# Performance work log

Hardware: AMD Instinct MI355X
Metric: run time of the kernel (lower is better)

The kernel has to match this reference:

```python
import jax, jax.numpy as jnp
import numpy as np

N = 40000   # num_words
H = 384     # hidden_dim
D = 20000   # num_docs
E = 800000  # word-word edges
NNZ = 800000  # doc-word tfidf entries
ALPHA = 0.65
EPS = 1e-5


def layernorm(x, g, b):
    m = jnp.mean(x, axis=-1, keepdims=True)
    v = jnp.mean((x - m) ** 2, axis=-1, keepdims=True)
    return (x - m) * jax.lax.rsqrt(v + EPS) * g + b


def gelu(x):
    return jax.nn.gelu(x, approximate=False)  # torch F.gelu default (erf)


def spmm(rows, cols, vals, M, n_out):
    # COO sparse [n_out, n_in] @ dense [n_in, H]
    return jax.ops.segment_sum(vals[:, None] * M[cols], rows, num_segments=n_out)


def setup_inputs() -> dict:
    key = jax.random.key(0)
    ks = jax.random.split(key, 24)
    s = 1.0 / np.sqrt(H)
    inp = {
        "A_rows": jax.random.randint(ks[0], (E,), 0, N, dtype=jnp.int32),
        "A_cols": jax.random.randint(ks[1], (E,), 0, N, dtype=jnp.int32),
        "A_vals": jax.random.uniform(ks[2], (E,), jnp.float32),
        "X_rows": jax.random.randint(ks[3], (NNZ,), 0, D, dtype=jnp.int32),
        "X_cols": jax.random.randint(ks[4], (NNZ,), 0, N, dtype=jnp.int32),
        "X_vals": jax.random.uniform(ks[5], (NNZ,), jnp.float32),
        "num_docs": D,
        "emb": jax.random.normal(ks[6], (N, H), jnp.float32) * s,
        "W1": jax.random.normal(ks[7], (H, H), jnp.float32) * s,
        "W2": jax.random.normal(ks[8], (H, H), jnp.float32) * s,
        "W3": jax.random.normal(ks[9], (H, H), jnp.float32) * s,
        "g1": jnp.ones((H,), jnp.float32), "b1": jnp.zeros((H,), jnp.float32),
        "g2": jnp.ones((H,), jnp.float32), "b2": jnp.zeros((H,), jnp.float32),
        "g3": jnp.ones((H,), jnp.float32), "b3": jnp.zeros((H,), jnp.float32),
        "mlp_W1": jax.random.normal(ks[10], (H, H), jnp.float32) * s,
        "mlp_b1": jnp.zeros((H,), jnp.float32),
        "mlp_g": jnp.ones((H,), jnp.float32), "mlp_bn": jnp.zeros((H,), jnp.float32),
        "mlp_W2": jax.random.normal(ks[11], (H, H // 2), jnp.float32) * s,
        "mlp_b2": jnp.zeros((H // 2,), jnp.float32),
        "cls_W": jax.random.normal(ks[12], (H // 2, 2), jnp.float32) * s,
        "cls_b": jnp.zeros((2,), jnp.float32),
        "gate_W1": jax.random.normal(ks[13], (2 * H, H), jnp.float32) * s,
        "gate_b1": jnp.zeros((H,), jnp.float32),
        "gate_W2": jax.random.normal(ks[14], (H, H), jnp.float32) * s,
        "gate_b2": jnp.zeros((H,), jnp.float32),
    }
    return inp


def reference(A_rows, A_cols, A_vals, X_rows, X_cols, X_vals, num_docs, emb,
              W1, W2, W3, g1, b1, g2, b2, g3, b3,
              mlp_W1, mlp_b1, mlp_g, mlp_bn, mlp_W2, mlp_b2,
              cls_W, cls_b, gate_W1, gate_b1, gate_W2, gate_b2):
    n = emb.shape[0]
    # --- 3 residual GCN blocks over word graph (eval mode: dropout off) ---
    h = spmm(A_rows, A_cols, A_vals, emb, n)
    h = gelu(layernorm(h @ W1, g1, b1))
    h = spmm(A_rows, A_cols, A_vals, h, n)
    h = gelu(layernorm(h @ W2, g2, b2))
    h = spmm(A_rows, A_cols, A_vals, h, n)
    h = gelu(layernorm(h @ W3, g3, b3))
    word_H = (1.0 - ALPHA) * emb + ALPHA * h
    # --- doc aggregation via TF-IDF SpMM ---
    doc_H = spmm(X_rows, X_cols, X_vals, word_H, num_docs)
    doc_H0 = spmm(X_rows, X_cols, X_vals, emb, num_docs)
    gate_in = jnp.concatenate([doc_H, doc_H0], axis=1)
    gate = jax.nn.sigmoid(gelu(gate_in @ gate_W1 + gate_b1) @ gate_W2 + gate_b2)
    doc = gate * doc_H + (1.0 - gate) * doc_H0
    # --- MLP head ---
    doc = layernorm(gelu(doc @ mlp_W1 + mlp_b1), mlp_g, mlp_bn)
    doc = gelu(doc @ mlp_W2 + mlp_b2)
    logits = doc @ cls_W + cls_b
    return logits
```

## Files before the change

### kernel.cpp

```cpp
#include <hip/hip_runtime.h>
#include <hip/hip_fp16.h>

#define HD 384
#define HHD 192
#define TPR 96
#define RPB 4
#define ECHUNK 128

using bf16x8 = __attribute__((ext_vector_type(8))) short;
using f32x4  = __attribute__((ext_vector_type(4))) float;

__device__ __forceinline__ float gelu_f(float x) {
    return 0.5f * x * (1.0f + erff(x * 0.70710678118654752f));
}

__device__ __forceinline__ float sigmoid_f(float x) {
    return 1.0f / (1.0f + expf(-x));
}

__device__ __forceinline__ void ld_h4(const __half2* p, float2& lo, float2& hi) {
    uint2 raw = *reinterpret_cast<const uint2*>(p);
    lo = __half22float2(*reinterpret_cast<const __half2*>(&raw.x));
    hi = __half22float2(*reinterpret_cast<const __half2*>(&raw.y));
}

__global__ __launch_bounds__(256) void hist_rows(
        const int* __restrict__ rows, int* __restrict__ cnt, int nnz) {
    int e = blockIdx.x * blockDim.x + threadIdx.x;
    if (e < nnz) atomicAdd(&cnt[rows[e]], 1);
}

__global__ __launch_bounds__(256) void scan_local(
        const int* __restrict__ cnt, int* __restrict__ rp,
        int* __restrict__ bsum, int n) {
    __shared__ int wsum[4];
    int i = blockIdx.x * 256 + threadIdx.x;
    int lane = threadIdx.x & 63, wv = threadIdx.x >> 6;
    int v = (i < n) ? cnt[i] : 0;
    int s = v;
    #pragma unroll
    for (int o = 1; o < 64; o <<= 1) {
        int t = __shfl_up(s, o);
        if (lane >= o) s += t;
    }
    if (lane == 63) wsum[wv] = s;
    __syncthreads();
    int woff = 0;
    for (int w = 0; w < wv; ++w) woff += wsum[w];
    if (i < n) rp[i] = woff + s - v;
    if (threadIdx.x == 255) bsum[blockIdx.x] = woff + s;
}

__global__ __launch_bounds__(256) void scan_bsums(
        const int* __restrict__ bsum, int* __restrict__ boff,
        int nb, int* __restrict__ total_out) {
    __shared__ int tmp[256];
    int tid = threadIdx.x;
    int v = (tid < nb) ? bsum[tid] : 0;
    tmp[tid] = v;
    __syncthreads();
    for (int o = 1; o < 256; o <<= 1) {
        int t = (tid >= o) ? tmp[tid - o] : 0;
        __syncthreads();
        tmp[tid] += t;
        __syncthreads();
    }
    if (tid < nb) boff[tid] = tmp[tid] - v;
    if (tid == nb - 1) *total_out = tmp[tid];
}

__global__ __launch_bounds__(256) void scan_add(
        int* __restrict__ rp, const int* __restrict__ boff, int n) {
    int i = blockIdx.x * 256 + threadIdx.x;
    if (i < n) rp[i] += boff[i >> 8];
}

__global__ __launch_bounds__(256) void csr_scatter(
        const int* __restrict__ rows, const int* __restrict__ cols,
        const float* __restrict__ vals, const int* __restrict__ rp,
        int* __restrict__ fill, int* __restrict__ cp,
        float* __restrict__ vp, int nnz) {
    int e = blockIdx.x * blockDim.x + threadIdx.x;
    if (e >= nnz) return;
    int r = rows[e];
    int pos = rp[r] + atomicAdd(&fill[r], 1);
    cp[pos] = cols[e];
    vp[pos] = vals[e];
}

__global__ __launch_bounds__(256) void cvt_fp16(
        const float* __restrict__ in, __half2* __restrict__ out, int n2) {
    int i = blockIdx.x * blockDim.x + threadIdx.x;
    if (i >= n2) return;
    float2 v = reinterpret_cast<const float2*>(in)[i];
    out[i] = __floats2half2_rn(v.x, v.y);
}

__global__ __launch_bounds__(384) void spmm_h2(
        const int* __restrict__ rp, const int* __restrict__ cp,
        const float* __restrict__ vp, const __half2* __restrict__ in,
        __half2* __restrict__ out, int nrows) {
    __shared__ int   lc[RPB][ECHUNK];
    __shared__ float lv[RPB][ECHUNK];
    __shared__ int maxlen_s;
    const int rr = threadIdx.x / TPR;
    const int t  = threadIdx.x % TPR;
    const int r  = blockIdx.x * RPB + rr;
    int s = 0, len = 0;
    if (r < nrows) { s = rp[r]; len = rp[r + 1] - s; }
    if (threadIdx.x == 0) maxlen_s = 0;
    __syncthreads();
    if (t == 0) atomicMax(&maxlen_s, len);
    __syncthreads();
    const int nch = (maxlen_s + ECHUNK - 1) / ECHUNK;
    float a0 = 0.f, a1 = 0.f, a2 = 0.f, a3 = 0.f;
    for (int ch = 0; ch < nch; ++ch) {
        const int base = ch * ECHUNK;
        const int tile = min(ECHUNK, len - base);
        for (int i = t; i < tile; i += TPR) {
            lc[rr][i] = cp[s + base + i];
            lv[rr][i] = vp[s + base + i];
        }
        __syncthreads();
        int p = 0;
        for (; p + 4 <= tile; p += 4) {
            int   c0 = lc[rr][p],     c1 = lc[rr][p + 1];
            int   c2 = lc[rr][p + 2], c3 = lc[rr][p + 3];
            float v0 = lv[rr][p],     v1 = lv[rr][p + 1];
            float v2 = lv[rr][p + 2], v3 = lv[rr][p + 3];
            float2 x0l, x0h, x1l, x1h, x2l, x2h, x3l, x3h;
            ld_h4(in + (size_t)c0 * HHD + 2 * t, x0l, x0h);
            ld_h4(in + (size_t)c1 * HHD + 2 * t, x1l, x1h);
            ld_h4(in + (size_t)c2 * HHD + 2 * t, x2l, x2h);
            ld_h4(in + (size_t)c3 * HHD + 2 * t, x3l, x3h);
            a0 = fmaf(v0, x0l.x, a0); a1 = fmaf(v0, x0l.y, a1);
            a2 = fmaf(v0, x0h.x, a2); a3 = fmaf(v0, x0h.y, a3);
            a0 = fmaf(v1, x1l.x, a0); a1 = fmaf(v1, x1l.y, a1);
            a2 = fmaf(v1, x1h.x, a2); a3 = fmaf(v1, x1h.y, a3);
            a0 = fmaf(v2, x2l.x, a0); a1 = fmaf(v2, x2l.y, a1);
            a2 = fmaf(v2, x2h.x, a2); a3 = fmaf(v2, x2h.y, a3);
            a0 = fmaf(v3, x3l.x, a0); a1 = fmaf(v3, x3l.y, a1);
            a2 = fmaf(v3, x3h.x, a2); a3 = fmaf(v3, x3h.y, a3);
        }
        for (; p < tile; ++p) {
            int c = lc[rr][p];
            float v = lv[rr][p];
            float2 xl, xh;
            ld_h4(in + (size_t)c * HHD + 2 * t, xl, xh);
            a0 = fmaf(v, xl.x, a0); a1 = fmaf(v, xl.y, a1);
            a2 = fmaf(v, xh.x, a2); a3 = fmaf(v, xh.y, a3);
        }
        __syncthreads();
    }
    if (r < nrows) {
        __half2 o0 = __floats2half2_rn(a0, a1);
        __half2 o1 = __floats2half2_rn(a2, a3);
        uint2 packed;
        packed.x = *reinterpret_cast<unsigned*>(&o0);
        packed.y = *reinterpret_cast<unsigned*>(&o1);
        *reinterpret_cast<uint2*>(out + (size_t)r * HHD + 2 * t) = packed;
    }
}

__global__ __launch_bounds__(384) void spmm_doc2(
        const int* __restrict__ rp, const int* __restrict__ cp,
        const float* __restrict__ vp,
        const __half2* __restrict__ inH, const __half2* __restrict__ inE,
        float* __restrict__ docH, float* __restrict__ docH0, int nrows) {
    __shared__ int   lc[RPB][ECHUNK];
    __shared__ float lv[RPB][ECHUNK];
    __shared__ int maxlen_s;
    const int rr = threadIdx.x / TPR;
    const int t  = threadIdx.x % TPR;
    const int r  = blockIdx.x * RPB + rr;
    int s = 0, len = 0;
    if (r < nrows) { s = rp[r]; len = rp[r + 1] - s; }
    if (threadIdx.x == 0) maxlen_s = 0;
    __syncthreads();
    if (t == 0) atomicMax(&maxlen_s, len);
    __syncthreads();
    const int nch = (maxlen_s + ECHUNK - 1) / ECHUNK;
    float h0 = 0.f, h1 = 0.f, h2 = 0.f, h3 = 0.f;
    float e0 = 0.f, e1 = 0.f, e2 = 0.f, e3 = 0.f;
    for (int ch = 0; ch < nch; ++ch) {
        const int base = ch * ECHUNK;
        const int tile = min(ECHUNK, len - base);
        for (int i = t; i < tile; i += TPR) {
            lc[rr][i] = cp[s + base + i];
            lv[rr][i] = vp[s + base + i];
        }
        __syncthreads();
        int p = 0;
        for (; p + 2 <= tile; p += 2) {
            int   c0 = lc[rr][p], c1 = lc[rr][p + 1];
            float v0 = lv[rr][p], v1 = lv[rr][p + 1];
            float2 ha0, hb0, ea0, eb0, ha1, hb1, ea1, eb1;
            ld_h4(inH + (size_t)c0 * HHD + 2 * t, ha0, hb0);
            ld_h4(inE + (size_t)c0 * HHD + 2 * t, ea0, eb0);
            ld_h4(inH + (size_t)c1 * HHD + 2 * t, ha1, hb1);
            ld_h4(inE + (size_t)c1 * HHD + 2 * t, ea1, eb1);
            h0 = fmaf(v0, ha0.x, h0); h1 = fmaf(v0, ha0.y, h1);
            h2 = fmaf(v0, hb0.x, h2); h3 = fmaf(v0, hb0.y, h3);
            e0 = fmaf(v0, ea0.x, e0); e1 = fmaf(v0, ea0.y, e1);
            e2 = fmaf(v0, eb0.x, e2); e3 = fmaf(v0, eb0.y, e3);
            h0 = fmaf(v1, ha1.x, h0); h1 = fmaf(v1, ha1.y, h1);
            h2 = fmaf(v1, hb1.x, h2); h3 = fmaf(v1, hb1.y, h3);
            e0 = fmaf(v1, ea1.x, e0); e1 = fmaf(v1, ea1.y, e1);
            e2 = fmaf(v1, eb1.x, e2); e3 = fmaf(v1, eb1.y, e3);
        }
        for (; p < tile; ++p) {
            int c = lc[rr][p];
            float v = lv[rr][p];
            float2 ha, hb, ea, eb;
            ld_h4(inH + (size_t)c * HHD + 2 * t, ha, hb);
            ld_h4(inE + (size_t)c * HHD + 2 * t, ea, eb);
            h0 = fmaf(v, ha.x, h0); h1 = fmaf(v, ha.y, h1);
            h2 = fmaf(v, hb.x, h2); h3 = fmaf(v, hb.y, h3);
            e0 = fmaf(v, ea.x, e0); e1 = fmaf(v, ea.y, e1);
            e2 = fmaf(v, eb.x, e2); e3 = fmaf(v, eb.y, e3);
        }
        __syncthreads();
    }
    if (r < nrows) {
        float4 ev = make_float4(e0, e1, e2, e3);
        float4 hv = make_float4(0.35f * e0 + 0.65f * h0, 0.35f * e1 + 0.65f * h1,
                                0.35f * e2 + 0.65f * h2, 0.35f * e3 + 0.65f * h3);
        *reinterpret_cast<float4*>(docH0 + (size_t)r * HD + 4 * t) = ev;
        *reinterpret_cast<float4*>(docH  + (size_t)r * HD + 4 * t) = hv;
    }
}

__global__ __launch_bounds__(256) void pack_w(
        const float* __restrict__ W, unsigned short* __restrict__ out,
        int KS, int NS, int N) {
    int t = blockIdx.x * 256 + threadIdx.x;
    int total = KS * NS * 64;
    if (t >= total) return;
    int l = t & 63;
    int ns = (t >> 6) % NS;
    int ks = t / (64 * NS);
    int col = ns * 16 + (l & 15);
    int k0 = ks * 32 + 8 * (l >> 4);
    size_t obase = (size_t)t * 8;
    size_t pstride = (size_t)KS * NS * 512;
    #pragma unroll
    for (int e = 0; e < 8; ++e) {
        float f = W[(size_t)(k0 + e) * N + col];
        unsigned u = __float_as_uint(f);
        unsigned short h = (unsigned short)(u >> 16);
        float r = f - __uint_as_float(u & 0xFFFF0000u);
        unsigned short lo = (unsigned short)(__float_as_uint(r) >> 16);
        out[obase + e] = (unsigned short)h;
        out[pstride + obase + e] = lo;
    }
}

__device__ __forceinline__ void splitf(const float* f, bf16x8& h, bf16x8& l) {
    #pragma unroll
    for (int e = 0; e < 8; ++e) {
        unsigned u = __float_as_uint(f[e]);
        h[e] = (short)(unsigned short)(u >> 16);
        float r = f[e] - __uint_as_float(u & 0xFFFF0000u);
        l[e] = (short)(unsigned short)(__float_as_uint(r) >> 16);
    }
}

template<int MODE, int NS, int KS, int KSPLIT, bool A16, bool OUT16>
__global__ __launch_bounds__(256) void gemm_mfma(
        const float* __restrict__ A1, const float* __restrict__ A2,
        const unsigned short* __restrict__ Wp,
        const float* __restrict__ bias, const float* __restrict__ gamma,
        const float* __restrict__ beta,
        const float* __restrict__ aux1, const float* __restrict__ aux2,
        float* __restrict__ out, int M) {
    constexpr int N = NS * 16;
    constexpr int NSW = NS / 4;
    const int tid = threadIdx.x;
    const int wave = tid >> 6, l = tid & 63;
    const int row_base = blockIdx.x * 16;
    const int arow = row_base + (l & 15);
    const bool arow_ok = arow < M;
    const int koff = 8 * (l >> 4);
    const size_t pstride = (size_t)KS * NS * 512;

    __shared__ float ps[4][16], pq[4][16];
    __shared__ float mean_s[16], rstd_s[16];
    __shared__ float plg[4][16][2];

    f32x4 acc[NSW];
    #pragma unroll
    for (int ns = 0; ns < NSW; ++ns)
        acc[ns] = f32x4{0.f, 0.f, 0.f, 0.f};

    for (int ks = 0; ks < KS; ++ks) {
        const float* Ap;
        int ksl;
        if (ks < KSPLIT) { Ap = A1; ksl = ks; }
        else             { Ap = A2; ksl = ks - KSPLIT; }
        bf16x8 ah, al;
        if (arow_ok) {
            float f[8];
            if constexpr (A16) {
                const __half2* src = reinterpret_cast<const __half2*>(Ap)
                                     + ((size_t)arow * HD + ksl * 32 + koff) / 2;
                #pragma unroll
                for (int e = 0; e < 4; ++e) {
                    float2 v = __half22float2(src[e]);
                    f[2 * e]     = v.x;
                    f[2 * e + 1] = v.y;
                }
            } else {
                const float* src = Ap + (size_t)arow * HD + ksl * 32 + koff;
                float4 a0 = *reinterpret_cast<const float4*>(src);
                float4 a1 = *reinterpret_cast<const float4*>(src + 4);
                f[0] = a0.x; f[1] = a0.y; f[2] = a0.z; f[3] = a0.w;
                f[4] = a1.x; f[5] = a1.y; f[6] = a1.z; f[7] = a1.w;
            }
            splitf(f, ah, al);
        } else {
            #pragma unroll
            for (int e = 0; e < 8; ++e) { ah[e] = 0; al[e] = 0; }
        }
        const unsigned short* Bp = Wp + (size_t)ks * NS * 512
                                   + (size_t)wave * NSW * 512 + (size_t)l * 8;
        #pragma unroll
        for (int ns = 0; ns < NSW; ++ns) {
            bf16x8 bh = *reinterpret_cast<const bf16x8*>(Bp + ns * 512);
            bf16x8 bl = *reinterpret_cast<const bf16x8*>(Bp + pstride + ns * 512);
            acc[ns] = __builtin_amdgcn_mfma_f32_16x16x32_bf16(ah, bh, acc[ns], 0, 0, 0);
            acc[ns] = __builtin_amdgcn_mfma_f32_16x16x32_bf16(al, bh, acc[ns], 0, 0, 0);
            acc[ns] = __builtin_amdgcn_mfma_f32_16x16x32_bf16(ah, bl, acc[ns], 0, 0, 0);
        }
    }

    const int col_lane = l & 15;
    const int g4 = (l >> 4) * 4;
    constexpr float invN = 1.0f / (float)N;

    if constexpr (MODE == 0 || MODE == 3) {
        if constexpr (MODE == 3) {
            #pragma unroll
            for (int ns = 0; ns < NSW; ++ns) {
                float bb = bias[(wave * NSW + ns) * 16 + col_lane];
                #pragma unroll
                for (int r = 0; r < 4; ++r)
                    acc[ns][r] = gelu_f(acc[ns][r] + bb);
            }
        }
        float s[4] = {0.f, 0.f, 0.f, 0.f}, q[4] = {0.f, 0.f, 0.f, 0.f};
        #pragma unroll
        for (int ns = 0; ns < NSW; ++ns)
            #pragma unroll
            for (int r = 0; r < 4; ++r) {
                float v = acc[ns][r];
                s[r] += v;
                q[r] += v * v;
            }
        #pragma unroll
        for (int r = 0; r < 4; ++r) {
            #pragma unroll
            for (int m = 1; m < 16; m <<= 1) {
                s[r] += __shfl_xor(s[r], m);
                q[r] += __shfl_xor(q[r], m);
            }
        }
        if (col_lane == 0) {
            #pragma unroll
            for (int r = 0; r < 4; ++r) {
                ps[wave][g4 + r] = s[r];
                pq[wave][g4 + r] = q[r];
            }
        }
        __syncthreads();
        if (tid < 16) {
            float ss = ps[0][tid] + ps[1][tid] + ps[2][tid] + ps[3][tid];
            float qq = pq[0][tid] + pq[1][tid] + pq[2][tid] + pq[3][tid];
            float m = ss * invN;
            mean_s[tid] = m;
            rstd_s[tid] = rsqrtf(qq * invN - m * m + 1e-5f);
        }
        __syncthreads();
        #pragma unroll
        for (int ns = 0; ns < NSW; ++ns) {
            int col = (wave * NSW + ns) * 16 + col_lane;
            float gg = gamma[col], bb = beta[col];
            #pragma unroll
            for (int r = 0; r < 4; ++r) {
                int row = row_base + g4 + r;
                if (row < M) {
                    float y = (acc[ns][r] - mean_s[g4 + r]) * rstd_s[g4 + r] * gg + bb;
                    if constexpr (MODE == 0) {
                        y = gelu_f(y);
                        if constexpr (OUT16)
                            reinterpret_cast<__half*>(out)[(size_t)row * N + col] =
                                __float2half(y);
                        else
                            out[(size_t)row * N + col] = y;
                    } else {
                        out[(size_t)row * N + col] = y;
                    }
                }
            }
        }
    } else if constexpr (MODE == 1) {
        #pragma unroll
        for (int ns = 0; ns < NSW; ++ns) {
            int col = (wave * NSW + ns) * 16 + col_lane;
            float bb = bias[col];
            #pragma unroll
            for (int r = 0; r < 4; ++r) {
                int row = row_base + g4 + r;
                if (row < M)
                    out[(size_t)row * N + col] = gelu_f(acc[ns][r] + bb);
            }
        }
    } else if constexpr (MODE == 2) {
        #pragma unroll
        for (int ns = 0; ns < NSW; ++ns) {
            int col = (wave * NSW + ns) * 16 + col_lane;
            float bb = bias[col];
            #pragma unroll
            for (int r = 0; r < 4; ++r) {
                int row = row_base + g4 + r;
                if (row < M) {
                    float g = sigmoid_f(acc[ns][r] + bb);
                    float h1 = aux1[(size_t)row * N + col];
                    float h0 = aux2[(size_t)row * N + col];
                    out[(size_t)row * N + col] = g * h1 + (1.0f - g) * h0;
                }
            }
        }
    } else if constexpr (MODE == 4) {
        float lg0[4] = {0.f, 0.f, 0.f, 0.f}, lg1[4] = {0.f, 0.f, 0.f, 0.f};
        #pragma unroll
        for (int ns = 0; ns < NSW; ++ns) {
            int col = (wave * NSW + ns) * 16 + col_lane;
            float bb = bias[col];
            float c0 = aux1[col * 2 + 0];
            float c1 = aux1[col * 2 + 1];
            #pragma unroll
            for (int r = 0; r < 4; ++r) {
                float v = gelu_f(acc[ns][r] + bb);
                lg0[r] = fmaf(v, c0, lg0[r]);
                lg1[r] = fmaf(v, c1, lg1[r]);
            }
        }
        #pragma unroll
        for (int r = 0; r < 4; ++r) {
            #pragma unroll
            for (int m = 1; m < 16; m <<= 1) {
                lg0[r] += __shfl_xor(lg0[r], m);
                lg1[r] += __shfl_xor(lg1[r], m);
            }
        }
        if (col_lane == 0) {
            #pragma unroll
            for (int r = 0; r < 4; ++r) {
                plg[wave][g4 + r][0] = lg0[r];
                plg[wave][g4 + r][1] = lg1[r];
            }
        }
        __syncthreads();
        if (tid < 32) {
            int rloc = tid >> 1, c = tid & 1;
            int row = row_base + rloc;
            if (row < M) {
                float t = plg[0][rloc][c] + plg[1][rloc][c]
                        + plg[2][rloc][c] + plg[3][rloc][c];
                out[(size_t)row * 2 + c] = t + gamma[c];
            }
        }
    }
}

static void build_csr(const int* rows, const int* cols, const float* vals,
                      int nnz, int n, int* rp, int* cp, float* vp,
                      int* cnt, int* bsum, int* boff, hipStream_t stream) {
    hipMemsetAsync(cnt, 0, (size_t)n * sizeof(int), stream);
    hist_rows<<<(nnz + 255) / 256, 256, 0, stream>>>(rows, cnt, nnz);
    int nb = (n + 255) / 256;
    scan_local<<<nb, 256, 0, stream>>>(cnt, rp, bsum, n);
    scan_bsums<<<1, 256, 0, stream>>>(bsum, boff, nb, rp + n);
    scan_add<<<nb, 256, 0, stream>>>(rp, boff, n);
    hipMemsetAsync(cnt, 0, (size_t)n * sizeof(int), stream);
    csr_scatter<<<(nnz + 255) / 256, 256, 0, stream>>>(rows, cols, vals, rp, cnt, cp, vp, nnz);
}

extern "C" void kernel_launch(void* const* d_in, const int* in_sizes, int n_in,
                              void* d_out, int out_size, void* d_ws, size_t ws_size,
                              hipStream_t stream) {
    const int*   A_rows = (const int*)  d_in[0];
    const int*   A_cols = (const int*)  d_in[1];
    const float* A_vals = (const float*)d_in[2];
    const int*   X_rows = (const int*)  d_in[3];
    const int*   X_cols = (const int*)  d_in[4];
    const float* X_vals = (const float*)d_in[5];
    const float* emb    = (const float*)d_in[7];
    const float* W1     = (const float*)d_in[8];
    const float* W2     = (const float*)d_in[9];
    const float* W3     = (const float*)d_in[10];
    const float* g1     = (const float*)d_in[11];
    const float* b1     = (const float*)d_in[12];
    const float* g2     = (const float*)d_in[13];
    const float* b2     = (const float*)d_in[14];
    const float* g3     = (const float*)d_in[15];
    const float* b3     = (const float*)d_in[16];
    const float* mW1    = (const float*)d_in[17];
    const float* mb1    = (const float*)d_in[18];
    const float* mg     = (const float*)d_in[19];
    const float* mbn    = (const float*)d_in[20];
    const float* mW2    = (const float*)d_in[21];
    const float* mb2    = (const float*)d_in[22];
    const float* cW     = (const float*)d_in[23];
    const float* cb     = (const float*)d_in[24];
    const float* gW1    = (const float*)d_in[25];
    const float* gb1    = (const float*)d_in[26];
    const float* gW2    = (const float*)d_in[27];
    const float* gb2    = (const float*)d_in[28];

    const int E_   = in_sizes[0];
    const int NNZ_ = in_sizes[3];
    const int N_   = in_sizes[7] / HD;
    const int D_   = out_size / 2;

    __half2* emb16 = (__half2*)d_ws;
    __half2* Ba    = emb16 + (size_t)N_ * HHD;
    __half2* Bb    = Ba    + (size_t)N_ * HHD;
    float* docH0 = (float*)(Bb + (size_t)N_ * HHD);
    int*   A_rp = (int*)(docH0 + (size_t)D_ * HD);
    int*   A_cp = A_rp + (N_ + 1);
    float* A_vp = (float*)(A_cp + E_);
    int*   X_rp = (int*)(A_vp + E_);
    int*   X_cp = X_rp + (D_ + 1);
    float* X_vp = (float*)(X_cp + NNZ_);
    int*   cnt  = (int*)(X_vp + NNZ_);
    int*   bsum = cnt + N_;
    int*   boff = bsum + 256;
    size_t pk_off = ((size_t)(boff + 256 - (int*)d_ws) + 7) & ~(size_t)7;
    unsigned short* packs = (unsigned short*)((float*)d_ws + pk_off);
    const size_t SZ_SQ = (size_t)2 * HD * HD;
    unsigned short* p_W1  = packs;
    unsigned short* p_W2  = p_W1  + SZ_SQ;
    unsigned short* p_W3  = p_W2  + SZ_SQ;
    unsigned short* p_gW2 = p_W3  + SZ_SQ;
    unsigned short* p_mW1 = p_gW2 + SZ_SQ;
    unsigned short* p_gW1 = p_mW1 + SZ_SQ;
    unsigned short* p_mW2 = p_gW1 + (size_t)2 * 2 * HD * HD;

    float* docH  = (float*)Ba;
    float* t1    = (float*)emb16;
    float* dmix  = (float*)Bb;
    float* un    = (float*)Ba;
    float* logits = (float*)d_out;

    const int word_grid = (N_ + 15) / 16;
    const int doc_grid  = (D_ + 15) / 16;
    const int spmm_word_grid = (N_ + RPB - 1) / RPB;
    const int spmm_doc_grid  = (D_ + RPB - 1) / RPB;

    pack_w<<<(12 * 24 * 64 + 255) / 256, 256, 0, stream>>>(W1,  p_W1,  12, 24, HD);
    pack_w<<<(12 * 24 * 64 + 255) / 256, 256, 0, stream>>>(W2,  p_W2,  12, 24, HD);
    pack_w<<<(12 * 24 * 64 + 255) / 256, 256, 0, stream>>>(W3,  p_W3,  12, 24, HD);
    pack_w<<<(12 * 24 * 64 + 255) / 256, 256, 0, stream>>>(gW2, p_gW2, 12, 24, HD);
    pack_w<<<(12 * 24 * 64 + 255) / 256, 256, 0, stream>>>(mW1, p_mW1, 12, 24, HD);
    pack_w<<<(24 * 24 * 64 + 255) / 256, 256, 0, stream>>>(gW1, p_gW1, 24, 24, HD);
    pack_w<<<(12 * 12 * 64 + 255) / 256, 256, 0, stream>>>(mW2, p_mW2, 12, 12, HHD);

    cvt_fp16<<<((N_ * HHD) + 255) / 256, 256, 0, stream>>>(emb, emb16, N_ * HHD);

    build_csr(A_rows, A_cols, A_vals, E_, N_, A_rp, A_cp, A_vp, cnt, bsum, boff, stream);
    build_csr(X_rows, X_cols, X_vals, NNZ_, D_, X_rp, X_cp, X_vp, cnt, bsum, boff, stream);

    spmm_h2<<<spmm_word_grid, 384, 0, stream>>>(A_rp, A_cp, A_vp, emb16, Ba, N_);
    gemm_mfma<0, 24, 12, 12, true, true><<<word_grid, 256, 0, stream>>>(
        (const float*)Ba, nullptr, p_W1, nullptr, g1, b1, nullptr, nullptr, (float*)Bb, N_);
    spmm_h2<<<spmm_word_grid, 384, 0, stream>>>(A_rp, A_cp, A_vp, Bb, Ba, N_);
    gemm_mfma<0, 24, 12, 12, true, true><<<word_grid, 256, 0, stream>>>(
        (const float*)Ba, nullptr, p_W2, nullptr, g2, b2, nullptr, nullptr, (float*)Bb, N_);
    spmm_h2<<<spmm_word_grid, 384, 0, stream>>>(A_rp, A_cp, A_vp, Bb, Ba, N_);
    gemm_mfma<0, 24, 12, 12, true, true><<<word_grid, 256, 0, stream>>>(
        (const float*)Ba, nullptr, p_W3, nullptr, g3, b3, nullptr, nullptr, (float*)Bb, N_);

    spmm_doc2<<<spmm_doc_grid, 384, 0, stream>>>(X_rp, X_cp, X_vp, Bb, emb16,
                                                 docH, docH0, D_);

    gemm_mfma<1, 24, 24, 12, false, false><<<doc_grid, 256, 0, stream>>>(
        docH, docH0, p_gW1, gb1, nullptr, nullptr, nullptr, nullptr, t1, D_);
    gemm_mfma<2, 24, 12, 12, false, false><<<doc_grid, 256, 0, stream>>>(
        t1, nullptr, p_gW2, gb2, nullptr, nullptr, docH, docH0, dmix, D_);
    gemm_mfma<3, 24, 12, 12, false, false><<<doc_grid, 256, 0, stream>>>(
        dmix, nullptr, p_mW1, mb1, mg, mbn, nullptr, nullptr, un, D_);
    gemm_mfma<4, 12, 12, 12, false, false><<<doc_grid, 256, 0, stream>>>(
        un, nullptr, p_mW2, mb2, cb, nullptr, cW, nullptr, logits, D_);
}
```

Measured before the change: 1.129 ms.

## Process two 16-row M tiles per block in word-graph GEMMs to reuse B fragments

Adds an MT template parameter so each GEMM block computes MT 16-row tiles, sharing each loaded packed-weight fragment across several A tiles. The three word-graph GEMMs use MT=2 with half the grid, while the doc-side GEMMs stay at MT=1. This aims to halve weight-fragment global/L2 traffic per output row, at the cost of more accumulator registers (possible occupancy loss) and fewer blocks.

```diff
diff --git a/kernel.cpp b/kernel.cpp
--- a/kernel.cpp
+++ b/kernel.cpp
@@ -265,7 +265,30 @@
     }
 }
 
-template<int MODE, int NS, int KS, int KSPLIT, bool A16, bool OUT16>
+template<bool A16>
+__device__ __forceinline__ void load_afrag(
+        const float* Ap, int arow, int ksl, int koff, bf16x8& ah, bf16x8& al) {
+    float f[8];
+    if constexpr (A16) {
+        const __half2* src = reinterpret_cast<const __half2*>(Ap)
+                             + ((size_t)arow * HD + ksl * 32 + koff) / 2;
+        #pragma unroll
+        for (int e = 0; e < 4; ++e) {
+            float2 v = __half22float2(src[e]);
+            f[2 * e]     = v.x;
+            f[2 * e + 1] = v.y;
+        }
+    } else {
+        const float* src = Ap + (size_t)arow * HD + ksl * 32 + koff;
+        float4 a0 = *reinterpret_cast<const float4*>(src);
+        float4 a1 = *reinterpret_cast<const float4*>(src + 4);
+        f[0] = a0.x; f[1] = a0.y; f[2] = a0.z; f[3] = a0.w;
+        f[4] = a1.x; f[5] = a1.y; f[6] = a1.z; f[7] = a1.w;
+    }
+    splitf(f, ah, al);
+}
+
+template<int MODE, int NS, int KS, int KSPLIT, bool A16, bool OUT16, int MT>
 __global__ __launch_bounds__(256) void gemm_mfma(
         const float* __restrict__ A1, const float* __restrict__ A2,
         const unsigned short* __restrict__ Wp,
@@ -277,49 +300,43 @@
     constexpr int NSW = NS / 4;
     const int tid = threadIdx.x;
     const int wave = tid >> 6, l = tid & 63;
-    const int row_base = blockIdx.x * 16;
-    const int arow = row_base + (l & 15);
-    const bool arow_ok = arow < M;
+    const int row_base = blockIdx.x * (16 * MT);
     const int koff = 8 * (l >> 4);
     const size_t pstride = (size_t)KS * NS * 512;
 
-    __shared__ float ps[4][16], pq[4][16];
-    __shared__ float mean_s[16], rstd_s[16];
-    __shared__ float plg[4][16][2];
-
-    f32x4 acc[NSW];
+    __shared__ float ps[4][16 * MT], pq[4][16 * MT];
+    __shared__ float mean_s[16 * MT], rstd_s[16 * MT];
+    __shared__ float plg[4][16 * MT][2];
+
+    int arow[MT];
+    bool aok[MT];
     #pragma unroll
-    for (int ns = 0; ns < NSW; ++ns)
-        acc[ns] = f32x4{0.f, 0.f, 0.f, 0.f};
+    for (int mt = 0; mt < MT; ++mt) {
+        arow[mt] = row_base + mt * 16 + (l & 15);
+        aok[mt] = arow[mt] < M;
+    }
+
+    f32x4 acc[MT][NSW];
+    #pragma unroll
+    for (int mt = 0; mt < MT; ++mt)
+        #pragma unroll
+        for (int ns = 0; ns < NSW; ++ns)
+            acc[mt][ns] = f32x4{0.f, 0.f, 0.f, 0.f};
 
     for (int ks = 0; ks < KS; ++ks) {
         const float* Ap;
         int ksl;
         if (ks < KSPLIT) { Ap = A1; ksl = ks; }
         else             { Ap = A2; ksl = ks - KSPLIT; }
-        bf16x8 ah, al;
-        if (arow_ok) {
-            float f[8];
-            if constexpr (A16) {
-                const __half2* src = reinterpret_cast<const __half2*>(Ap)
-                                     + ((size_t)arow * HD + ksl * 32 + koff) / 2;
-                #pragma unroll
-                for (int e = 0; e < 4; ++e) {
-                    float2 v = __half22float2(src[e]);
-                    f[2 * e]     = v.x;
-                    f[2 * e + 1] = v.y;
-                }
+        bf16x8 ah[MT], al[MT];
+        #pragma unroll
+        for (int mt = 0; mt < MT; ++mt) {
+            if (aok[mt]) {
+                load_afrag<A16>(Ap, arow[mt], ksl, koff, ah[mt], al[mt]);
             } else {
-                const float* src = Ap + (size_t)arow * HD + ksl * 32 + koff;
-                float4 a0 = *reinterpret_cast<const float4*>(src);
-                float4 a1 = *reinterpret_cast<const float4*>(src + 4);
-                f[0] = a0.x; f[1] = a0.y; f[2] = a0.z; f[3] = a0.w;
-                f[4] = a1.x; f[5] = a1.y; f[6] = a1.z; f[7] = a1.w;
-            }
-            splitf(f, ah, al);
-        } else {
-            #pragma unroll
-            for (int e = 0; e < 8; ++e) { ah[e] = 0; al[e] = 0; }
+                #pragma unroll
+                for (int e = 0; e < 8; ++e) { ah[mt][e] = 0; al[mt][e] = 0; }
+            }
         }
         const unsigned short* Bp = Wp + (size_t)ks * NS * 512
                                    + (size_t)wave * NSW * 512 + (size_t)l * 8;
@@ -327,9 +344,12 @@
         for (int ns = 0; ns < NSW; ++ns) {
             bf16x8 bh = *reinterpret_cast<const bf16x8*>(Bp + ns * 512);
             bf16x8 bl = *reinterpret_cast<const bf16x8*>(Bp + pstride + ns * 512);
-            acc[ns] = __builtin_amdgcn_mfma_f32_16x16x32_bf16(ah, bh, acc[ns], 0, 0, 0);
-            acc[ns] = __builtin_amdgcn_mfma_f32_16x16x32_bf16(al, bh, acc[ns], 0, 0, 0);
-            acc[ns] = __builtin_amdgcn_mfma_f32_16x16x32_bf16(ah, bl, acc[ns], 0, 0, 0);
+            #pragma unroll
+            for (int mt = 0; mt < MT; ++mt) {
+                acc[mt][ns] = __builtin_amdgcn_mfma_f32_16x16x32_bf16(ah[mt], bh, acc[mt][ns], 0, 0, 0);
+                acc[mt][ns] = __builtin_amdgcn_mfma_f32_16x16x32_bf16(al[mt], bh, acc[mt][ns], 0, 0, 0);
+                acc[mt][ns] = __builtin_amdgcn_mfma_f32_16x16x32_bf16(ah[mt], bl, acc[mt][ns], 0, 0, 0);
+            }
         }
     }
 
@@ -340,39 +360,44 @@
     if constexpr (MODE == 0 || MODE == 3) {
         if constexpr (MODE == 3) {
             #pragma unroll
-            for (int ns = 0; ns < NSW; ++ns) {
-                float bb = bias[(wave * NSW + ns) * 16 + col_lane];
-                #pragma unroll
-                for (int r = 0; r < 4; ++r)
-                    acc[ns][r] = gelu_f(acc[ns][r] + bb);
-            }
-        }
-        float s[4] = {0.f, 0.f, 0.f, 0.f}, q[4] = {0.f, 0.f, 0.f, 0.f};
-        #pragma unroll
-        for (int ns = 0; ns < NSW; ++ns)
+            for (int mt = 0; mt < MT; ++mt)
+                #pragma unroll
+                for (int ns = 0; ns < NSW; ++ns) {
+                    float bb = bias[(wave * NSW + ns) * 16 + col_lane];
+                    #pragma unroll
+                    for (int r = 0; r < 4; ++r)
+                        acc[mt][ns][r] = gelu_f(acc[mt][ns][r] + bb);
+                }
+        }
+        #pragma unroll
+        for (int mt = 0; mt < MT; ++mt) {
+            float s[4] = {0.f, 0.f, 0.f, 0.f}, q[4] = {0.f, 0.f, 0.f, 0.f};
+            #pragma unroll
+            for (int ns = 0; ns < NSW; ++ns)
+                #pragma unroll
+                for (int r = 0; r < 4; ++r) {
+                    float v = acc[mt][ns][r];
+                    s[r] += v;
+                    q[r] += v * v;
+                }
             #pragma unroll
             for (int r = 0; r < 4; ++r) {
-                float v = acc[ns][r];
-                s[r] += v;
-                q[r] += v * v;
-            }
-        #pragma unroll
-        for (int r = 0; r < 4; ++r) {
-            #pragma unroll
-            for (int m = 1; m < 16; m <<= 1) {
-                s[r] += __shfl_xor(s[r], m);
-                q[r] += __shfl_xor(q[r], m);
-            }
-        }
-        if (col_lane == 0) {
-            #pragma unroll
-            for (int r = 0; r < 4; ++r) {
-                ps[wave][g4 + r] = s[r];
-                pq[wave][g4 + r] = q[r];
-            }
-        }
-        __syncthreads();
-        if (tid < 16) {
+                #pragma unroll
+                for (int m = 1; m < 16; m <<= 1) {
+                    s[r] += __shfl_xor(s[r], m);
+                    q[r] += __shfl_xor(q[r], m);
+                }
+            }
+            if (col_lane == 0) {
+                #pragma unroll
+                for (int r = 0; r < 4; ++r) {
+                    ps[wave][mt * 16 + g4 + r] = s[r];
+                    pq[wave][mt * 16 + g4 + r] = q[r];
+                }
+            }
+        }
+        __syncthreads();
+        if (tid < 16 * MT) {
             float ss = ps[0][tid] + ps[1][tid] + ps[2][tid] + ps[3][tid];
             float qq = pq[0][tid] + pq[1][tid] + pq[2][tid] + pq[3][tid];
             float m = ss * invN;
@@ -381,87 +406,97 @@
         }
         __syncthreads();
         #pragma unroll
-        for (int ns = 0; ns < NSW; ++ns) {
-            int col = (wave * NSW + ns) * 16 + col_lane;
-            float gg = gamma[col], bb = beta[col];
+        for (int mt = 0; mt < MT; ++mt)
+            #pragma unroll
+            for (int ns = 0; ns < NSW; ++ns) {
+                int col = (wave * NSW + ns) * 16 + col_lane;
+                float gg = gamma[col], bb = beta[col];
+                #pragma unroll
+                for (int r = 0; r < 4; ++r) {
+                    int lidx = mt * 16 + g4 + r;
+                    int row = row_base + lidx;
+                    if (row < M) {
+                        float y = (acc[mt][ns][r] - mean_s[lidx]) * rstd_s[lidx] * gg + bb;
+                        if constexpr (MODE == 0) {
+                            y = gelu_f(y);
+                            if constexpr (OUT16)
+                                reinterpret_cast<__half*>(out)[(size_t)row * N + col] =
+                                    __float2half(y);
+                            else
+                                out[(size_t)row * N + col] = y;
+                        } else {
+                            out[(size_t)row * N + col] = y;
+                        }
+                    }
+                }
+            }
+    } else if constexpr (MODE == 1) {
+        #pragma unroll
+        for (int mt = 0; mt < MT; ++mt)
+            #pragma unroll
+            for (int ns = 0; ns < NSW; ++ns) {
+                int col = (wave * NSW + ns) * 16 + col_lane;
+                float bb = bias[col];
+                #pragma unroll
+                for (int r = 0; r < 4; ++r) {
+                    int row = row_base + mt * 16 + g4 + r;
+                    if (row < M)
+                        out[(size_t)row * N + col] = gelu_f(acc[mt][ns][r] + bb);
+                }
+            }
+    } else if constexpr (MODE == 2) {
+        #pragma unroll
+        for (int mt = 0; mt < MT; ++mt)
+            #pragma unroll
+            for (int ns = 0; ns < NSW; ++ns) {
+                int col = (wave * NSW + ns) * 16 + col_lane;
+                float bb = bias[col];
+                #pragma unroll
+                for (int r = 0; r < 4; ++r) {
+                    int row = row_base + mt * 16 + g4 + r;
+                    if (row < M) {
+                        float g = sigmoid_f(acc[mt][ns][r] + bb);
+                        float h1 = aux1[(size_t)row * N + col];
+                        float h0 = aux2[(size_t)row * N + col];
+                        out[(size_t)row * N + col] = g * h1 + (1.0f - g) * h0;
+                    }
+                }
+            }
+    } else if constexpr (MODE == 4) {
+        #pragma unroll
+        for (int mt = 0; mt < MT; ++mt) {
+            float lg0[4] = {0.f, 0.f, 0.f, 0.f}, lg1[4] = {0.f, 0.f, 0.f, 0.f};
+            #pragma unroll
+            for (int ns = 0; ns < NSW; ++ns) {
+                int col = (wave * NSW + ns) * 16 + col_lane;
+                float bb = bias[col];
+                float c0 = aux1[col * 2 + 0];
+                float c1 = aux1[col * 2 + 1];
+                #pragma unroll
+                for (int r = 0; r < 4; ++r) {
+                    float v = gelu_f(acc[mt][ns][r] + bb);
+                    lg0[r] = fmaf(v, c0, lg0[r]);
+                    lg1[r] = fmaf(v, c1, lg1[r]);
+                }
+            }
             #pragma unroll
             for (int r = 0; r < 4; ++r) {
-                int row = row_base + g4 + r;
-                if (row < M) {
-                    float y = (acc[ns][r] - mean_s[g4 + r]) * rstd_s[g4 + r] * gg + bb;
-                    if constexpr (MODE == 0) {
-                        y = gelu_f(y);
-                        if constexpr (OUT16)
-                            reinterpret_cast<__half*>(out)[(size_t)row * N + col] =
-                                __float2half(y);
-                        else
-                            out[(size_t)row * N + col] = y;
-                    } else {
-                        out[(size_t)row * N + col] = y;
-                    }
-                }
-            }
-        }
-    } else if constexpr (MODE == 1) {
-        #pragma unroll
-        for (int ns = 0; ns < NSW; ++ns) {
-            int col = (wave * NSW + ns) * 16 + col_lane;
-            float bb = bias[col];
-            #pragma unroll
-            for (int r = 0; r < 4; ++r) {
-                int row = row_base + g4 + r;
-                if (row < M)
-                    out[(size_t)row * N + col] = gelu_f(acc[ns][r] + bb);
-            }
-        }
-    } else if constexpr (MODE == 2) {
-        #pragma unroll
-        for (int ns = 0; ns < NSW; ++ns) {
-            int col = (wave * NSW + ns) * 16 + col_lane;
-            float bb = bias[col];
-            #pragma unroll
-            for (int r = 0; r < 4; ++r) {
-                int row = row_base + g4 + r;
-                if (row < M) {
-                    float g = sigmoid_f(acc[ns][r] + bb);
-                    float h1 = aux1[(size_t)row * N + col];
-                    float h0 = aux2[(size_t)row * N + col];
-                    out[(size_t)row * N + col] = g * h1 + (1.0f - g) * h0;
-                }
-            }
-        }
-    } else if constexpr (MODE == 4) {
-        float lg0[4] = {0.f, 0.f, 0.f, 0.f}, lg1[4] = {0.f, 0.f, 0.f, 0.f};
-        #pragma unroll
-        for (int ns = 0; ns < NSW; ++ns) {
-            int col = (wave * NSW + ns) * 16 + col_lane;
-            float bb = bias[col];
-            float c0 = aux1[col * 2 + 0];
-            float c1 = aux1[col * 2 + 1];
-            #pragma unroll
-            for (int r = 0; r < 4; ++r) {
-                float v = gelu_f(acc[ns][r] + bb);
-                lg0[r] = fmaf(v, c0, lg0[r]);
-                lg1[r] = fmaf(v, c1, lg1[r]);
-            }
-        }
-        #pragma unroll
-        for (int r = 0; r < 4; ++r) {
-            #pragma unroll
-            for (int m = 1; m < 16; m <<= 1) {
-                lg0[r] += __shfl_xor(lg0[r], m);
-                lg1[r] += __shfl_xor(lg1[r], m);
-            }
-        }
-        if (col_lane == 0) {
-            #pragma unroll
-            for (int r = 0; r < 4; ++r) {
-                plg[wave][g4 + r][0] = lg0[r];
-                plg[wave][g4 + r][1] = lg1[r];
-            }
-        }
-        __syncthreads();
-        if (tid < 32) {
+                #pragma unroll
+                for (int m = 1; m < 16; m <<= 1) {
+                    lg0[r] += __shfl_xor(lg0[r], m);
+                    lg1[r] += __shfl_xor(lg1[r], m);
+                }
+            }
+            if (col_lane == 0) {
+                #pragma unroll
+                for (int r = 0; r < 4; ++r) {
+                    plg[wave][mt * 16 + g4 + r][0] = lg0[r];
+                    plg[wave][mt * 16 + g4 + r][1] = lg1[r];
+                }
+            }
+        }
+        __syncthreads();
+        if (tid < 32 * MT) {
             int rloc = tid >> 1, c = tid & 1;
             int row = row_base + rloc;
             if (row < M) {
@@ -553,7 +588,7 @@
     float* un    = (float*)Ba;
     float* logits = (float*)d_out;
 
-    const int word_grid = (N_ + 15) / 16;
+    const int word_grid = (N_ + 31) / 32;
     const int doc_grid  = (D_ + 15) / 16;
     const int spmm_word_grid = (N_ + RPB - 1) / RPB;
     const int spmm_doc_grid  = (D_ + RPB - 1) / RPB;
@@ -572,24 +607,24 @@
     build_csr(X_rows, X_cols, X_vals, NNZ_, D_, X_rp, X_cp, X_vp, cnt, bsum, boff, stream);
 
     spmm_h2<<<spmm_word_grid, 384, 0, stream>>>(A_rp, A_cp, A_vp, emb16, Ba, N_);
-    gemm_mfma<0, 24, 12, 12, true, true><<<word_grid, 256, 0, stream>>>(
+    gemm_mfma<0, 24, 12, 12, true, true, 2><<<word_grid, 256, 0, stream>>>(
         (const float*)Ba, nullptr, p_W1, nullptr, g1, b1, nullptr, nullptr, (float*)Bb, N_);
     spmm_h2<<<spmm_word_grid, 384, 0, stream>>>(A_rp, A_cp, A_vp, Bb, Ba, N_);
-    gemm_mfma<0, 24, 12, 12, true, true><<<word_grid, 256, 0, stream>>>(
+    gemm_mfma<0, 24, 12, 12, true, true, 2><<<word_grid, 256, 0, stream>>>(
         (const float*)Ba, nullptr, p_W2, nullptr, g2, b2, nullptr, nullptr, (float*)Bb, N_);
     spmm_h2<<<spmm_word_grid, 384, 0, stream>>>(A_rp, A_cp, A_vp, Bb, Ba, N_);
-    gemm_mfma<0, 24, 12, 12, true, true><<<word_grid, 256, 0, stream>>>(
+    gemm_mfma<0, 24, 12, 12, true, true, 2><<<word_grid, 256, 0, stream>>>(
         (const float*)Ba, nullptr, p_W3, nullptr, g3, b3, nullptr, nullptr, (float*)Bb, N_);
 
     spmm_doc2<<<spmm_doc_grid, 384, 0, stream>>>(X_rp, X_cp, X_vp, Bb, emb16,
                                                  docH, docH0, D_);
 
-    gemm_mfma<1, 24, 24, 12, false, false><<<doc_grid, 256, 0, stream>>>(
+    gemm_mfma<1, 24, 24, 12, false, false, 1><<<doc_grid, 256, 0, stream>>>(
         docH, docH0, p_gW1, gb1, nullptr, nullptr, nullptr, nullptr, t1, D_);
-    gemm_mfma<2, 24, 12, 12, false, false><<<doc_grid, 256, 0, stream>>>(
+    gemm_mfma<2, 24, 12, 12, false, false, 1><<<doc_grid, 256, 0, stream>>>(
         t1, nullptr, p_gW2, gb2, nullptr, nullptr, docH, docH0, dmix, D_);
-    gemm_mfma<3, 24, 12, 12, false, false><<<doc_grid, 256, 0, stream>>>(
+    gemm_mfma<3, 24, 12, 12, false, false, 1><<<doc_grid, 256, 0, stream>>>(
         dmix, nullptr, p_mW1, mb1, mg, mbn, nullptr, nullptr, un, D_);
-    gemm_mfma<4, 12, 12, 12, false, false><<<doc_grid, 256, 0, stream>>>(
+    gemm_mfma<4, 12, 12, 12, false, false, 1><<<doc_grid, 256, 0, stream>>>(
         un, nullptr, p_mW2, mb2, cb, nullptr, cW, nullptr, logits, D_);
 }
```

Measured after the change: 1.148 ms. Within noise of the previous version (+1.7%).
